# Optimization experiments

Hardware: AMD Instinct MI355X
Metric: run time of the kernel (lower is better)

Reference implementation:

```python
import jax, jax.numpy as jnp
import numpy as np

N_STOCKS = 5
SPD_DIM = N_STOCKS * (N_STOCKS + 1) // 2  # 15
STATE_DIM = N_STOCKS * N_STOCKS           # 25
CTX_DIM = 64
HIDDEN = 128
N_STEPS = 5
DT = 0.2
DIFFUSION_SCALE = 1.0
B = 4096
T = 32


def _spd_basis(n):
    bs = []
    for i in range(n):
        e = np.zeros((n, n), np.float32); e[i, i] = 1.0; bs.append(e)
    for i in range(n):
        for j in range(i + 1, n):
            e = np.zeros((n, n), np.float32)
            e[i, j] = e[j, i] = 1.0 / np.sqrt(2.0)
            bs.append(e)
    return jnp.asarray(np.stack(bs))  # (d, n, n) orthonormal symmetric basis

BASIS = _spd_basis(N_STOCKS)


def _sym(x):
    return 0.5 * (x + jnp.swapaxes(x, -1, -2))


def setup_inputs() -> dict:
    key = jax.random.key(0)
    ks = jax.random.split(key, 20)
    S, C, H, D = STATE_DIM, CTX_DIM, HIDDEN, SPD_DIM
    raw = jax.random.normal(ks[0], (B, T, N_STOCKS, N_STOCKS), jnp.float32)
    context_spd = raw @ jnp.swapaxes(raw, -1, -2) / N_STOCKS + jnp.eye(N_STOCKS, dtype=jnp.float32)
    dW = jax.random.normal(ks[1], (B, N_STEPS, D), jnp.float32) * jnp.sqrt(DT).astype(jnp.float32)

    def lin(k, out_d, in_d, scale=1.0):
        return jax.random.normal(k, (out_d, in_d), jnp.float32) * (scale / np.sqrt(in_d))

    inp_d = S + C  # 89
    return {
        "context_spd": context_spd,
        "dW": dW,
        "gru_wih": lin(ks[2], 3 * H, S),
        "gru_whh": lin(ks[3], 3 * H, H),
        "gru_bias": jnp.zeros((3 * H,), jnp.float32),
        "gru_bias_n": jnp.zeros((H,), jnp.float32),
        "proj_w": lin(ks[4], C, H),
        "proj_b": jnp.zeros((C,), jnp.float32),
        "drift_w0": lin(ks[5], H, inp_d), "drift_b0": jnp.zeros((H,), jnp.float32),
        "drift_w1": lin(ks[6], H, H),    "drift_b1": jnp.zeros((H,), jnp.float32),
        "drift_w2": lin(ks[7], H, H),    "drift_b2": jnp.zeros((H,), jnp.float32),
        "drift_w3": lin(ks[8], D, H) * 0.001, "drift_b3": jnp.zeros((D,), jnp.float32),
        "diff_w0": lin(ks[9], H, inp_d), "diff_b0": jnp.zeros((H,), jnp.float32),
        "diff_w1": lin(ks[10], H, H),   "diff_b1": jnp.zeros((H,), jnp.float32),
        "diff_w2": lin(ks[11], D, H) * 0.001, "diff_b2": jnp.full((D,), -3.0, jnp.float32),
    }


def reference(context_spd, dW, gru_wih, gru_whh, gru_bias, gru_bias_n, proj_w, proj_b,
              drift_w0, drift_b0, drift_w1, drift_b1, drift_w2, drift_b2, drift_w3, drift_b3,
              diff_w0, diff_b0, diff_w1, diff_b1, diff_w2, diff_b2):
    b = context_spd.shape[0]
    n = context_spd.shape[-1]

    # ---- GRU encoder over flattened symmetrized SPD matrices ----
    feats = _sym(context_spd).reshape(b, context_spd.shape[1], n * n)  # (B, T, S)

    def gru_step(h, x):  # x: (B, S), h: (B, H)
        gi = x @ gru_wih.T + gru_bias
        gh = h @ gru_whh.T
        ir, iz, ig = jnp.split(gi, 3, axis=-1)
        hr, hz, hg = jnp.split(gh, 3, axis=-1)
        r = jax.nn.sigmoid(ir + hr)
        z = jax.nn.sigmoid(iz + hz)
        g = jnp.tanh(ig + r * (hg + gru_bias_n))
        return (1.0 - z) * g + z * h, None

    h0 = jnp.zeros((b, gru_whh.shape[1]), feats.dtype)
    hT, _ = jax.lax.scan(gru_step, h0, jnp.swapaxes(feats, 0, 1))
    ctx = hT @ proj_w.T + proj_b  # (B, ctx_dim)

    # ---- SPD geometry helpers (affine-invariant frame) ----
    def sqrtm_sym(sig):
        w, v = jnp.linalg.eigh(sig)
        w = jnp.clip(w, 1e-8, None)
        return (v * jnp.sqrt(w)[..., None, :]) @ jnp.swapaxes(v, -1, -2)

    def expm_sym(a):
        w, v = jnp.linalg.eigh(a)
        return (v * jnp.exp(w)[..., None, :]) @ jnp.swapaxes(v, -1, -2)

    # ---- geometric Euler-Maruyama SDE step ----
    def sde_step(sigma, dw):  # sigma: (B,n,n), dw: (B,d)
        state = _sym(sigma).reshape(b, -1)
        inp = jnp.concatenate([state, ctx], axis=-1)  # (B, 89)
        # drift MLP (depth 3: 4 linears, silu)
        h = jax.nn.silu(inp @ drift_w0.T + drift_b0)
        h = jax.nn.silu(h @ drift_w1.T + drift_b1)
        h = jax.nn.silu(h @ drift_w2.T + drift_b2)
        drift_c = h @ drift_w3.T + drift_b3  # (B, d)
        # diffusion MLP (depth 2: 3 linears, silu), softplus-scaled
        g = jax.nn.silu(inp @ diff_w0.T + diff_b0)
        g = jax.nn.silu(g @ diff_w1.T + diff_b1)
        scales = jax.nn.softplus(g @ diff_w2.T + diff_b2) * DIFFUSION_SCALE  # (B, d)
        coeff = drift_c * DT + scales * dw  # tangent coordinates in orthonormal frame
        a = jnp.einsum('bk,kij->bij', coeff, BASIS)  # symmetric (B,n,n)
        L = sqrtm_sym(_sym(sigma))  # symmetric sqrt; frame E_k = L B_k L
        sigma_new = L @ expm_sym(a) @ L  # exp map: L expm(L^-1 V L^-1) L
        return _sym(sigma_new), None

    y0 = _sym(context_spd[:, -1])
    yT, _ = jax.lax.scan(sde_step, y0, jnp.swapaxes(dW, 0, 1))
    return _sym(yT)
```

## Files before the change

kernel.cpp:

```cpp
#include <hip/hip_runtime.h>
#include <hip/hip_bf16.h>

typedef unsigned int uint;

#define T_STEPS 32

#define OFF_WB    0
#define OFF_PJB   30720
#define OFF_D0B   34816
#define OFF_D1B   40960
#define OFF_D2B   49152
#define OFF_G0B   57344
#define OFF_G1B   63488
#define OFF_W3B   71680
#define OFF_G2B   72704

typedef _Float16 half8 __attribute__((ext_vector_type(8)));
typedef float    f32x4 __attribute__((ext_vector_type(4)));

union FB { uint4 u4; half8 h; };

__device__ inline uint pack2f(float a, float b) {
  _Float16 ha = (_Float16)a, hb = (_Float16)b;
  unsigned short ua, ub;
  __builtin_memcpy(&ua, &ha, 2);
  __builtin_memcpy(&ub, &hb, 2);
  return (uint)ua | ((uint)ub << 16);
}

__device__ inline float sigm(float x) { return 1.f / (1.f + __expf(-x)); }
__device__ inline float tanh_f(float x) {
  float ax = fabsf(x);
  float e = __expf(2.f * ax);
  float t = 1.f - 2.f / (e + 1.f);
  return copysignf(t, x);
}
__device__ inline float silu_f(float x) { return x / (1.f + __expf(-x)); }

__device__ inline float map89(const float* __restrict__ W, int u, int k) {
  if (k < 25) return W[u * 89 + k];
  if (k < 32) return 0.f;
  return W[u * 89 + k - 7];
}

__global__ __launch_bounds__(256) void prep_kernel(
    const float* __restrict__ wih, const float* __restrict__ whh,
    const float* __restrict__ pw,
    const float* __restrict__ dw0, const float* __restrict__ dw1,
    const float* __restrict__ dw2, const float* __restrict__ gw0,
    const float* __restrict__ gw1, const float* __restrict__ dw3,
    const float* __restrict__ gw2, uint* __restrict__ wsu) {
  int id = blockIdx.x * 256 + threadIdx.x;
  if (id < 30720) {
    int i = id & 3, l = (id >> 2) & 63, t3 = id >> 8;
    int kt = t3 % 5, wg = t3 / 5;
    int w = wg / 3, gi = wg % 3;
    int row = gi * 128 + w * 16 + (l & 15);
    int k = ((l >> 4) << 3) + i * 2;
    float a, b;
    if (kt == 0) {
      a = (k     < 25) ? wih[row * 25 + k]     : 0.f;
      b = (k + 1 < 25) ? wih[row * 25 + k + 1] : 0.f;
    } else {
      int kh = (kt - 1) * 32 + k;
      a = whh[row * 128 + kh];
      b = whh[row * 128 + kh + 1];
    }
    wsu[OFF_WB + id] = pack2f(a, b);
  } else if (id < 34816) {
    int t = id - 30720;
    int i = t & 3, l = (t >> 2) & 63, wkt = t >> 8;
    int kt = wkt & 3, w = wkt >> 2;
    int u = w * 16 + (l & 15);
    int k = kt * 32 + ((l >> 4) << 3) + i * 2;
    wsu[OFF_PJB + t] = pack2f(pw[u * 128 + k], pw[u * 128 + k + 1]);
  } else if (id < 40960) {
    int t = id - 34816;
    int i = t & 3, l = (t >> 2) & 63, wkt = t >> 8;
    int kt = wkt % 3, w = wkt / 3;
    int u = w * 16 + (l & 15);
    int k = kt * 32 + ((l >> 4) << 3) + i * 2;
    wsu[OFF_D0B + t] = pack2f(map89(dw0, u, k), map89(dw0, u, k + 1));
  } else if (id < 49152) {
    int t = id - 40960;
    int i = t & 3, l = (t >> 2) & 63, wkt = t >> 8;
    int kt = wkt & 3, w = wkt >> 2;
    int u = w * 16 + (l & 15);
    int k = kt * 32 + ((l >> 4) << 3) + i * 2;
    wsu[OFF_D1B + t] = pack2f(dw1[u * 128 + k], dw1[u * 128 + k + 1]);
  } else if (id < 57344) {
    int t = id - 49152;
    int i = t & 3, l = (t >> 2) & 63, wkt = t >> 8;
    int kt = wkt & 3, w = wkt >> 2;
    int u = w * 16 + (l & 15);
    int k = kt * 32 + ((l >> 4) << 3) + i * 2;
    wsu[OFF_D2B + t] = pack2f(dw2[u * 128 + k], dw2[u * 128 + k + 1]);
  } else if (id < 63488) {
    int t = id - 57344;
    int i = t & 3, l = (t >> 2) & 63, wkt = t >> 8;
    int kt = wkt % 3, w = wkt / 3;
    int u = w * 16 + (l & 15);
    int k = kt * 32 + ((l >> 4) << 3) + i * 2;
    wsu[OFF_G0B + t] = pack2f(map89(gw0, u, k), map89(gw0, u, k + 1));
  } else if (id < 71680) {
    int t = id - 63488;
    int i = t & 3, l = (t >> 2) & 63, wkt = t >> 8;
    int kt = wkt & 3, w = wkt >> 2;
    int u = w * 16 + (l & 15);
    int k = kt * 32 + ((l >> 4) << 3) + i * 2;
    wsu[OFF_G1B + t] = pack2f(gw1[u * 128 + k], gw1[u * 128 + k + 1]);
  } else if (id < 72704) {
    int t = id - 71680;
    int i = t & 3, l = (t >> 2) & 63, kt = t >> 8;
    int o = l & 15;
    int k = kt * 32 + ((l >> 4) << 3) + i * 2;
    float a = (o < 15) ? dw3[o * 128 + k]     : 0.f;
    float b = (o < 15) ? dw3[o * 128 + k + 1] : 0.f;
    wsu[OFF_W3B + t] = pack2f(a, b);
  } else if (id < 73728) {
    int t = id - 72704;
    int i = t & 3, l = (t >> 2) & 63, kt = t >> 8;
    int o = l & 15;
    int k = kt * 32 + ((l >> 4) << 3) + i * 2;
    float a = (o < 15) ? gw2[o * 128 + k]     : 0.f;
    float b = (o < 15) ? gw2[o * 128 + k + 1] : 0.f;
    wsu[OFF_G2B + t] = pack2f(a, b);
  }
}

template <int KT>
__device__ inline void mlp_pair(const _Float16* __restrict__ aA,
                                const FB* B0, const FB* B1,
                                float bias0, float bias1,
                                _Float16* __restrict__ outA,
                                int lm, int lq, int ubase) {
  f32x4 c0 = {0.f, 0.f, 0.f, 0.f}, c1 = {0.f, 0.f, 0.f, 0.f};
#pragma unroll
  for (int kt = 0; kt < KT; kt++) {
    half8 a = *(const half8*)(aA + ((kt * 4 + lq) * 16 + lm) * 8);
    c0 = __builtin_amdgcn_mfma_f32_16x16x32_f16(a, B0[kt].h, c0, 0, 0, 0);
    c1 = __builtin_amdgcn_mfma_f32_16x16x32_f16(a, B1[kt].h, c1, 0, 0, 0);
  }
  int u0 = ubase + lm, u1 = ubase + 16 + lm;
  int base0 = (u0 >> 3) * 128 + (u0 & 7);
  int base1 = (u1 >> 3) * 128 + (u1 & 7);
#pragma unroll
  for (int s = 0; s < 4; s++) {
    outA[base0 + (lq * 4 + s) * 8] = (_Float16)silu_f(c0[s] + bias0);
    outA[base1 + (lq * 4 + s) * 8] = (_Float16)silu_f(c1[s] + bias1);
  }
}

__device__ inline f32x4 head4(const _Float16* __restrict__ aA, const FB* H,
                              int lm, int lq) {
  f32x4 c = {0.f, 0.f, 0.f, 0.f};
#pragma unroll
  for (int kt = 0; kt < 4; kt++) {
    half8 a = *(const half8*)(aA + ((kt * 4 + lq) * 16 + lm) * 8);
    c = __builtin_amdgcn_mfma_f32_16x16x32_f16(a, H[kt].h, c, 0, 0, 0);
  }
  return c;
}

__device__ inline float bpf(int addr, float v) {
  return __int_as_float(__builtin_amdgcn_ds_bpermute(addr, __float_as_int(v)));
}
__device__ inline float mm5b(int iA, int iB, float A, float B) {
  float c = 0.f;
#pragma unroll
  for (int k = 0; k < 5; k++)
    c = fmaf(bpf(iA + 4 * k, A), bpf(iB + 20 * k, B), c);
  return c;
}

#define NS_ITER do { \
  float P_  = mm5b(iA0, iB0, Zv, Yv); \
  float Tm_ = 1.5f * gdel - 0.5f * P_; \
  float Yn_ = mm5b(iA0, iB0, Yv, Tm_); \
  float Zn_ = mm5b(iA0, iB0, Tm_, Zv); \
  Yv = Yn_; Zv = Zn_; } while (0)

__global__ __launch_bounds__(512) void fused_kernel(
    const float* __restrict__ ctp, const float* __restrict__ dWp,
    const uint* __restrict__ wsu,
    const float* __restrict__ gbias, const float* __restrict__ gbn,
    const float* __restrict__ projb,
    const float* __restrict__ db0, const float* __restrict__ db1,
    const float* __restrict__ db2, const float* __restrict__ b3,
    const float* __restrict__ gb0, const float* __restrict__ gb1,
    const float* __restrict__ gb2, float* __restrict__ outp) {
  __shared__ __align__(16) _Float16 bigbuf[16384];
  __shared__ __align__(16) _Float16 hf[2][4][4][16][8];
  __shared__ float sig_s[16 * 28];
  __shared__ float coeff_s[256];
  __shared__ float coeff2_s[256];
  const int tid = threadIdx.x;
  const int rb = blockIdx.x * 16;
  uint* bigu = (uint*)bigbuf;

  for (int idx = tid; idx < T_STEPS * 16 * 16; idx += 512) {
    int k2 = idx & 15, r = (idx >> 4) & 15, t = idx >> 8;
    const float* base = ctp + ((rb + r) * T_STEPS + t) * 25;
    int k0 = 2 * k2;
    float v0 = 0.f, v1 = 0.f;
    if (k0 < 25)     { int i5 = k0 / 5,     j5 = k0 % 5;     v0 = 0.5f * (base[i5*5+j5] + base[j5*5+i5]); }
    if (k0 + 1 < 25) { int i5 = (k0+1) / 5, j5 = (k0+1) % 5; v1 = 0.5f * (base[i5*5+j5] + base[j5*5+i5]); }
    int q = k2 >> 2, jh = k2 & 3;
    bigu[((t * 4 + q) * 16 + r) * 4 + jh] = pack2f(v0, v1);
  }

  const int w = tid >> 6, l = tid & 63;
  const int lm = l & 15, lq = l >> 4;
  const int u = w * 16 + lm;
  const int ku = u >> 5, qu = (u >> 3) & 3, ju = u & 7;
  FB Bf[3][5];
  const uint4* wb4p = (const uint4*)(wsu + OFF_WB);
#pragma unroll
  for (int gi = 0; gi < 3; gi++)
#pragma unroll
    for (int kt = 0; kt < 5; kt++)
      Bf[gi][kt].u4 = wb4p[((w * 3 + gi) * 5 + kt) * 64 + l];
  const float br = gbias[u], bz = gbias[128 + u], bg = gbias[256 + u], bn = gbn[u];
  float hprev[4] = {0.f, 0.f, 0.f, 0.f};
  __syncthreads();

  f32x4 z4 = {0.f, 0.f, 0.f, 0.f};
  half8 axn = *(const half8*)(bigbuf + ((0 * 4 + lq) * 16 + lm) * 8);
  f32x4 pxr = __builtin_amdgcn_mfma_f32_16x16x32_f16(axn, Bf[0][0].h, z4, 0, 0, 0);
  f32x4 pxz = __builtin_amdgcn_mfma_f32_16x16x32_f16(axn, Bf[1][0].h, z4, 0, 0, 0);
  f32x4 pxg = __builtin_amdgcn_mfma_f32_16x16x32_f16(axn, Bf[2][0].h, z4, 0, 0, 0);
  for (int t = 0; t < T_STEPS; t++) {
    f32x4 cr = pxr, cz = pxz, cgv = pxg;
    f32x4 ch = {0.f, 0.f, 0.f, 0.f};
    if (t > 0) {
      const int p = t & 1;
#pragma unroll
      for (int kk = 0; kk < 4; kk++) {
        half8 ah = *(const half8*)(&hf[p][kk][lq][lm][0]);
        cr = __builtin_amdgcn_mfma_f32_16x16x32_f16(ah, Bf[0][1 + kk].h, cr, 0, 0, 0);
        cz = __builtin_amdgcn_mfma_f32_16x16x32_f16(ah, Bf[1][1 + kk].h, cz, 0, 0, 0);
        ch = __builtin_amdgcn_mfma_f32_16x16x32_f16(ah, Bf[2][1 + kk].h, ch, 0, 0, 0);
      }
    }
    if (t < T_STEPS - 1) {
      axn = *(const half8*)(bigbuf + (((t + 1) * 4 + lq) * 16 + lm) * 8);
      pxr = __builtin_amdgcn_mfma_f32_16x16x32_f16(axn, Bf[0][0].h, z4, 0, 0, 0);
      pxz = __builtin_amdgcn_mfma_f32_16x16x32_f16(axn, Bf[1][0].h, z4, 0, 0, 0);
      pxg = __builtin_amdgcn_mfma_f32_16x16x32_f16(axn, Bf[2][0].h, z4, 0, 0, 0);
    }
    const int wp = (t + 1) & 1;
#pragma unroll
    for (int s = 0; s < 4; s++) {
      float r = sigm(cr[s] + br);
      float z = sigm(cz[s] + bz);
      float g = tanh_f(cgv[s] + bg + r * (ch[s] + bn));
      float hn = (1.f - z) * g + z * hprev[s];
      hprev[s] = hn;
      hf[wp][ku][qu][lq * 4 + s][ju] = (_Float16)hn;
    }
    __syncthreads();
  }

  const int role = w >> 2;
  const int wbq = w & 3;
  FB F0[2][3], F1[2][4], F2[2][4], Pf[4], Hf[4];
  {
    const uint4* p0 = (const uint4*)(wsu + (role ? OFF_G0B : OFF_D0B));
    const uint4* p1 = (const uint4*)(wsu + (role ? OFF_G1B : OFF_D1B));
    const uint4* p2 = (const uint4*)(wsu + (role ? OFF_G1B : OFF_D2B));
#pragma unroll
    for (int s = 0; s < 2; s++) {
      int slot = wbq * 2 + s;
#pragma unroll
      for (int kt = 0; kt < 3; kt++) F0[s][kt].u4 = p0[(slot * 3 + kt) * 64 + l];
#pragma unroll
      for (int kt = 0; kt < 4; kt++) {
        F1[s][kt].u4 = p1[(slot * 4 + kt) * 64 + l];
        F2[s][kt].u4 = p2[(slot * 4 + kt) * 64 + l];
      }
    }
  }
  if (w < 4) {
#pragma unroll
    for (int kt = 0; kt < 4; kt++)
      Pf[kt].u4 = ((const uint4*)(wsu + OFF_PJB))[(w * 4 + kt) * 64 + l];
  }
  if (w == 0) {
#pragma unroll
    for (int kt = 0; kt < 4; kt++)
      Hf[kt].u4 = ((const uint4*)(wsu + OFF_W3B))[kt * 64 + l];
  } else if (w == 4) {
#pragma unroll
    for (int kt = 0; kt < 4; kt++)
      Hf[kt].u4 = ((const uint4*)(wsu + OFF_G2B))[kt * 64 + l];
  }
  float b0s[2], b1s[2], b2s[2];
#pragma unroll
  for (int s = 0; s < 2; s++) {
    int us = wbq * 32 + s * 16 + lm;
    b0s[s] = role ? gb0[us] : db0[us];
    b1s[s] = role ? gb1[us] : db1[us];
    b2s[s] = role ? 0.f : db2[us];
  }
  const int oc = (lm < 15) ? lm : 0;
  const float hb = (w == 0) ? b3[oc] : ((w == 4) ? gb2[oc] : 0.f);

  _Float16* inpA = bigbuf;
  _Float16* bufA = bigbuf + 1536;
  _Float16* bufB = bigbuf + 3584;
  _Float16* bufC = bigbuf + 5632;
  _Float16* bufD = bigbuf + 7680;

  if (w < 4) {
    f32x4 c = {0.f, 0.f, 0.f, 0.f};
#pragma unroll
    for (int kt = 0; kt < 4; kt++) {
      half8 a = *(const half8*)(&hf[0][kt][lq][lm][0]);
      c = __builtin_amdgcn_mfma_f32_16x16x32_f16(a, Pf[kt].h, c, 0, 0, 0);
    }
    const float pbv = projb[u];
    int kk = 32 + u, base = (kk >> 3) * 128 + (kk & 7);
#pragma unroll
    for (int s = 0; s < 4; s++)
      inpA[base + (lq * 4 + s) * 8] = (_Float16)(c[s] + pbv);
  }
  for (int idx = tid; idx < 400; idx += 512) {
    int e = idx / 25, k = idx % 25;
    int i5 = k / 5, j5 = k % 5;
    const float* base = ctp + ((rb + e) * T_STEPS + 31) * 25;
    float v = 0.5f * (base[i5 * 5 + j5] + base[j5 * 5 + i5]);
    sig_s[e * 28 + k] = v;
    inpA[(k >> 3) * 128 + e * 8 + (k & 7)] = (_Float16)v;
  }
  if (tid < 112) {
    int e = tid / 7, p = 25 + tid % 7;
    inpA[(p >> 3) * 128 + e * 8 + (p & 7)] = (_Float16)0.f;
  }
  const int ge = tid >> 5, glane = tid & 31;
  const int gli = (glane < 25) ? glane : 0;
  const int gii = gli / 5, gjj = gli % 5;
  const float gdel = (gii == gjj) ? 1.f : 0.f;
  const int gbase = (l & 32) << 2;
  const int iA0 = gbase + gii * 20;
  const int iB0 = gbase + gjj * 4;
  const int iT0 = gbase + (gjj * 5 + gii) * 4;
  __syncthreads();

  for (int st = 0; st < 5; st++) {
    float S = sig_s[ge * 28 + gli];
    float tr = 0.f;
#pragma unroll
    for (int d = 0; d < 5; d++) tr += bpf(gbase + 24 * d, S);
    const float That = S * (2.298851f / tr) - 1.068966f * gdel;
    float dwv[4] = {0.f, 0.f, 0.f, 0.f};
    if (w == 4) {
#pragma unroll
      for (int s = 0; s < 4; s++)
        dwv[s] = dWp[((rb + lq * 4 + s) * 5 + st) * 15 + oc];
    }
    float Yv, Zv;
    mlp_pair<3>(inpA, F0[0], F0[1], b0s[0], b0s[1], role ? bufB : bufA, lm, lq, wbq * 32);
    {
      float T2 = mm5b(iA0, iB0, That, That);
      float X  = -1.13859f * That + 0.9901f * T2;
      float Zp = mm5b(iA0, iB0, T2, X)
               + 1.03702f * gdel - 0.21179f * That + 0.09756f * T2;
      Zv = Zp;
      float TZ = mm5b(iA0, iB0, That, Zp);
      Yv = 0.87f * TZ + 0.93f * Zp;
    }
    __syncthreads();
    mlp_pair<4>(role ? bufB : bufA, F1[0], F1[1], b1s[0], b1s[1],
                role ? bufD : bufC, lm, lq, wbq * 32);
    NS_ITER;
    __syncthreads();
    if (!role) {
      mlp_pair<4>(bufC, F2[0], F2[1], b2s[0], b2s[1], bufA, lm, lq, wbq * 32);
    } else if (w == 4) {
      f32x4 c = head4(bufD, Hf, lm, lq);
      if (lm < 15) {
#pragma unroll
        for (int s = 0; s < 4; s++) {
          float acc = c[s] + hb;
          float sp = (acc > 20.f) ? acc : __logf(1.f + __expf(acc));
          coeff2_s[(lq * 4 + s) * 16 + lm] = sp * dwv[s];
        }
      }
    }
    NS_ITER;
    __syncthreads();
    if (w == 0) {
      f32x4 c = head4(bufA, Hf, lm, lq);
      if (lm < 15) {
#pragma unroll
        for (int s = 0; s < 4; s++)
          coeff_s[(lq * 4 + s) * 16 + lm] = 0.2f * (c[s] + hb);
      }
    }
    NS_ITER;
    float L = Yv * sqrtf(0.5f * tr);
    __syncthreads();
    {
      float av;
      if (gii == gjj) av = coeff_s[ge * 16 + gii] + coeff2_s[ge * 16 + gii];
      else {
        int p = gii < gjj ? gii : gjj, qq = gii < gjj ? gjj : gii;
        int i5 = 5 + (p * (9 - p)) / 2 + (qq - p - 1);
        av = (coeff_s[ge * 16 + i5] + coeff2_s[ge * 16 + i5]) * 0.70710678f;
      }
      float a2 = mm5b(iA0, iB0, av, av);
      float a3 = mm5b(iA0, iB0, a2, av);
      float q1 = gdel * 0.16666667f + av * 0.04166667f
               + a2 * 0.00833333f + a3 * 0.00138889f;
      float M = gdel + av + 0.5f * a2 + mm5b(iA0, iB0, a3, q1);
      float P2 = mm5b(iA0, iB0, L, M);
      float S2 = mm5b(iA0, iB0, P2, L);
      S2 = 0.5f * (S2 + bpf(iT0, S2));
      if (glane < 25) {
        sig_s[ge * 28 + gli] = S2;
        inpA[(gli >> 3) * 128 + ge * 8 + (gli & 7)] = (_Float16)S2;
      }
    }
    __syncthreads();
  }

  for (int idx = tid; idx < 400; idx += 512) {
    int e = idx / 25, k = idx % 25;
    outp[(rb + e) * 25 + k] = sig_s[e * 28 + k];
  }
}

extern "C" void kernel_launch(void* const* d_in, const int* in_sizes, int n_in,
                              void* d_out, int out_size, void* d_ws, size_t ws_size,
                              hipStream_t stream) {
  const float* ctp = (const float*)d_in[0];
  const float* dWp = (const float*)d_in[1];
  const float* wih = (const float*)d_in[2];
  const float* whh = (const float*)d_in[3];
  const float* gb  = (const float*)d_in[4];
  const float* gbn = (const float*)d_in[5];
  const float* pw  = (const float*)d_in[6];
  const float* pb  = (const float*)d_in[7];
  const float* dw0 = (const float*)d_in[8];
  const float* db0 = (const float*)d_in[9];
  const float* dw1 = (const float*)d_in[10];
  const float* db1 = (const float*)d_in[11];
  const float* dw2 = (const float*)d_in[12];
  const float* db2 = (const float*)d_in[13];
  const float* dw3 = (const float*)d_in[14];
  const float* db3 = (const float*)d_in[15];
  const float* gw0 = (const float*)d_in[16];
  const float* gb0 = (const float*)d_in[17];
  const float* gw1 = (const float*)d_in[18];
  const float* gb1 = (const float*)d_in[19];
  const float* gw2 = (const float*)d_in[20];
  const float* gb2 = (const float*)d_in[21];
  uint* wsu = (uint*)d_ws;

  hipLaunchKernelGGL(prep_kernel, dim3(288), dim3(256), 0, stream,
                     wih, whh, pw, dw0, dw1, dw2, gw0, gw1, dw3, gw2, wsu);
  hipLaunchKernelGGL(fused_kernel, dim3(256), dim3(512), 0, stream,
                     ctp, dWp, wsu, gb, gbn, pb,
                     db0, db1, db2, db3, gb0, gb1, gb2, (float*)d_out);
}
```

Baseline: 174.8 us.

## Split fused kernel into GRU and SDE kernels, halve SDE tile, use dot2 heads

The single fused kernel is split in two. A GRU kernel keeps 16 rows per 512-thread block and writes the fp16 context projection to workspace. A new SDE kernel runs 8 rows per 256-thread block over twice as many blocks, with each wave computing four output slices instead of two. The small drift and diffusion output heads now use packed fp16 dot2 instructions from weights held in LDS, replacing the single-wave MFMA heads, and one barrier is removed. The aim is better CU occupancy and less serial head work in the SDE phase, at the cost of an extra launch, a global round trip for the context, and more registers per wave.

```diff
diff --git a/kernel.cpp b/kernel.cpp
--- a/kernel.cpp
+++ b/kernel.cpp
@@ -12,9 +12,11 @@
 #define OFF_D2B   49152
 #define OFF_G0B   57344
 #define OFF_G1B   63488
-#define OFF_W3B   71680
-#define OFF_G2B   72704
-
+#define OFF_W3P   71680
+#define OFF_G2P   72640
+#define OFF_CTXG  73600
+
+typedef _Float16 h2v  __attribute__((ext_vector_type(2)));
 typedef _Float16 half8 __attribute__((ext_vector_type(8)));
 typedef float    f32x4 __attribute__((ext_vector_type(4)));
 
@@ -27,6 +29,22 @@
   __builtin_memcpy(&ub, &hb, 2);
   return (uint)ua | ((uint)ub << 16);
 }
+
+__device__ inline float dot2(uint w, uint a, float acc) {
+#if __has_builtin(__builtin_amdgcn_fdot2)
+  union U { uint u; h2v h; };
+  U uw, ua; uw.u = w; ua.u = a;
+  return __builtin_amdgcn_fdot2(uw.h, ua.h, acc, false);
+#else
+  union U { uint u; _Float16 h[2]; };
+  U uw, ua; uw.u = w; ua.u = a;
+  return acc + (float)uw.h[0] * (float)ua.h[0] + (float)uw.h[1] * (float)ua.h[1];
+#endif
+}
+
+#define DOT4(accv, wv, xv)                                             \
+  accv = dot2((wv).x, (xv).x, accv); accv = dot2((wv).y, (xv).y, accv);\
+  accv = dot2((wv).z, (xv).z, accv); accv = dot2((wv).w, (xv).w, accv);
 
 __device__ inline float sigm(float x) { return 1.f / (1.f + __expf(-x)); }
 __device__ inline float tanh_f(float x) {
@@ -109,94 +127,26 @@
     int u = w * 16 + (l & 15);
     int k = kt * 32 + ((l >> 4) << 3) + i * 2;
     wsu[OFF_G1B + t] = pack2f(gw1[u * 128 + k], gw1[u * 128 + k + 1]);
-  } else if (id < 72704) {
+  } else if (id < 72640) {
     int t = id - 71680;
-    int i = t & 3, l = (t >> 2) & 63, kt = t >> 8;
-    int o = l & 15;
-    int k = kt * 32 + ((l >> 4) << 3) + i * 2;
-    float a = (o < 15) ? dw3[o * 128 + k]     : 0.f;
-    float b = (o < 15) ? dw3[o * 128 + k + 1] : 0.f;
-    wsu[OFF_W3B + t] = pack2f(a, b);
-  } else if (id < 73728) {
-    int t = id - 72704;
-    int i = t & 3, l = (t >> 2) & 63, kt = t >> 8;
-    int o = l & 15;
-    int k = kt * 32 + ((l >> 4) << 3) + i * 2;
-    float a = (o < 15) ? gw2[o * 128 + k]     : 0.f;
-    float b = (o < 15) ? gw2[o * 128 + k + 1] : 0.f;
-    wsu[OFF_G2B + t] = pack2f(a, b);
-  }
-}
-
-template <int KT>
-__device__ inline void mlp_pair(const _Float16* __restrict__ aA,
-                                const FB* B0, const FB* B1,
-                                float bias0, float bias1,
-                                _Float16* __restrict__ outA,
-                                int lm, int lq, int ubase) {
-  f32x4 c0 = {0.f, 0.f, 0.f, 0.f}, c1 = {0.f, 0.f, 0.f, 0.f};
-#pragma unroll
-  for (int kt = 0; kt < KT; kt++) {
-    half8 a = *(const half8*)(aA + ((kt * 4 + lq) * 16 + lm) * 8);
-    c0 = __builtin_amdgcn_mfma_f32_16x16x32_f16(a, B0[kt].h, c0, 0, 0, 0);
-    c1 = __builtin_amdgcn_mfma_f32_16x16x32_f16(a, B1[kt].h, c1, 0, 0, 0);
-  }
-  int u0 = ubase + lm, u1 = ubase + 16 + lm;
-  int base0 = (u0 >> 3) * 128 + (u0 & 7);
-  int base1 = (u1 >> 3) * 128 + (u1 & 7);
-#pragma unroll
-  for (int s = 0; s < 4; s++) {
-    outA[base0 + (lq * 4 + s) * 8] = (_Float16)silu_f(c0[s] + bias0);
-    outA[base1 + (lq * 4 + s) * 8] = (_Float16)silu_f(c1[s] + bias1);
-  }
-}
-
-__device__ inline f32x4 head4(const _Float16* __restrict__ aA, const FB* H,
-                              int lm, int lq) {
-  f32x4 c = {0.f, 0.f, 0.f, 0.f};
-#pragma unroll
-  for (int kt = 0; kt < 4; kt++) {
-    half8 a = *(const half8*)(aA + ((kt * 4 + lq) * 16 + lm) * 8);
-    c = __builtin_amdgcn_mfma_f32_16x16x32_f16(a, H[kt].h, c, 0, 0, 0);
-  }
-  return c;
-}
-
-__device__ inline float bpf(int addr, float v) {
-  return __int_as_float(__builtin_amdgcn_ds_bpermute(addr, __float_as_int(v)));
-}
-__device__ inline float mm5b(int iA, int iB, float A, float B) {
-  float c = 0.f;
-#pragma unroll
-  for (int k = 0; k < 5; k++)
-    c = fmaf(bpf(iA + 4 * k, A), bpf(iB + 20 * k, B), c);
-  return c;
-}
-
-#define NS_ITER do { \
-  float P_  = mm5b(iA0, iB0, Zv, Yv); \
-  float Tm_ = 1.5f * gdel - 0.5f * P_; \
-  float Yn_ = mm5b(iA0, iB0, Yv, Tm_); \
-  float Zn_ = mm5b(iA0, iB0, Tm_, Zv); \
-  Yv = Yn_; Zv = Zn_; } while (0)
-
-__global__ __launch_bounds__(512) void fused_kernel(
-    const float* __restrict__ ctp, const float* __restrict__ dWp,
-    const uint* __restrict__ wsu,
+    int o = t >> 6, k2 = t & 63;
+    wsu[OFF_W3P + t] = pack2f(dw3[o * 128 + 2 * k2], dw3[o * 128 + 2 * k2 + 1]);
+  } else if (id < 73600) {
+    int t = id - 72640;
+    int o = t >> 6, k2 = t & 63;
+    wsu[OFF_G2P + t] = pack2f(gw2[o * 128 + 2 * k2], gw2[o * 128 + 2 * k2 + 1]);
+  }
+}
+
+__global__ __launch_bounds__(512) void gru_kernel(
+    const float* __restrict__ ctp, const uint* __restrict__ wsu,
     const float* __restrict__ gbias, const float* __restrict__ gbn,
-    const float* __restrict__ projb,
-    const float* __restrict__ db0, const float* __restrict__ db1,
-    const float* __restrict__ db2, const float* __restrict__ b3,
-    const float* __restrict__ gb0, const float* __restrict__ gb1,
-    const float* __restrict__ gb2, float* __restrict__ outp) {
-  __shared__ __align__(16) _Float16 bigbuf[16384];
+    const float* __restrict__ projb, _Float16* __restrict__ ctxg) {
+  __shared__ __align__(16) _Float16 x2[T_STEPS][4][16][8];
   __shared__ __align__(16) _Float16 hf[2][4][4][16][8];
-  __shared__ float sig_s[16 * 28];
-  __shared__ float coeff_s[256];
-  __shared__ float coeff2_s[256];
   const int tid = threadIdx.x;
   const int rb = blockIdx.x * 16;
-  uint* bigu = (uint*)bigbuf;
+  uint* x2u = (uint*)x2;
 
   for (int idx = tid; idx < T_STEPS * 16 * 16; idx += 512) {
     int k2 = idx & 15, r = (idx >> 4) & 15, t = idx >> 8;
@@ -206,7 +156,7 @@
     if (k0 < 25)     { int i5 = k0 / 5,     j5 = k0 % 5;     v0 = 0.5f * (base[i5*5+j5] + base[j5*5+i5]); }
     if (k0 + 1 < 25) { int i5 = (k0+1) / 5, j5 = (k0+1) % 5; v1 = 0.5f * (base[i5*5+j5] + base[j5*5+i5]); }
     int q = k2 >> 2, jh = k2 & 3;
-    bigu[((t * 4 + q) * 16 + r) * 4 + jh] = pack2f(v0, v1);
+    x2u[((t * 4 + q) * 16 + r) * 4 + jh] = pack2f(v0, v1);
   }
 
   const int w = tid >> 6, l = tid & 63;
@@ -225,7 +175,7 @@
   __syncthreads();
 
   f32x4 z4 = {0.f, 0.f, 0.f, 0.f};
-  half8 axn = *(const half8*)(bigbuf + ((0 * 4 + lq) * 16 + lm) * 8);
+  half8 axn = *(const half8*)(&x2[0][lq][lm][0]);
   f32x4 pxr = __builtin_amdgcn_mfma_f32_16x16x32_f16(axn, Bf[0][0].h, z4, 0, 0, 0);
   f32x4 pxz = __builtin_amdgcn_mfma_f32_16x16x32_f16(axn, Bf[1][0].h, z4, 0, 0, 0);
   f32x4 pxg = __builtin_amdgcn_mfma_f32_16x16x32_f16(axn, Bf[2][0].h, z4, 0, 0, 0);
@@ -243,7 +193,7 @@
       }
     }
     if (t < T_STEPS - 1) {
-      axn = *(const half8*)(bigbuf + (((t + 1) * 4 + lq) * 16 + lm) * 8);
+      axn = *(const half8*)(&x2[t + 1][lq][lm][0]);
       pxr = __builtin_amdgcn_mfma_f32_16x16x32_f16(axn, Bf[0][0].h, z4, 0, 0, 0);
       pxz = __builtin_amdgcn_mfma_f32_16x16x32_f16(axn, Bf[1][0].h, z4, 0, 0, 0);
       pxg = __builtin_amdgcn_mfma_f32_16x16x32_f16(axn, Bf[2][0].h, z4, 0, 0, 0);
@@ -261,16 +211,124 @@
     __syncthreads();
   }
 
-  const int role = w >> 2;
-  const int wbq = w & 3;
-  FB F0[2][3], F1[2][4], F2[2][4], Pf[4], Hf[4];
+  if (w < 4) {
+    FB Pf[4];
+#pragma unroll
+    for (int kt = 0; kt < 4; kt++)
+      Pf[kt].u4 = ((const uint4*)(wsu + OFF_PJB))[(w * 4 + kt) * 64 + l];
+    f32x4 c = {0.f, 0.f, 0.f, 0.f};
+#pragma unroll
+    for (int kt = 0; kt < 4; kt++) {
+      half8 a = *(const half8*)(&hf[0][kt][lq][lm][0]);
+      c = __builtin_amdgcn_mfma_f32_16x16x32_f16(a, Pf[kt].h, c, 0, 0, 0);
+    }
+    const float pbv = projb[u];
+#pragma unroll
+    for (int s = 0; s < 4; s++)
+      ctxg[(rb + lq * 4 + s) * 64 + u] = (_Float16)(c[s] + pbv);
+  }
+}
+
+template <int KT>
+__device__ inline void mlp_pair(const _Float16* __restrict__ aA,
+                                const FB* B0, const FB* B1,
+                                float bias0, float bias1,
+                                _Float16* __restrict__ outA,
+                                int lm, int lq, int ubase) {
+  f32x4 c0 = {0.f, 0.f, 0.f, 0.f}, c1 = {0.f, 0.f, 0.f, 0.f};
+#pragma unroll
+  for (int kt = 0; kt < KT; kt++) {
+    half8 a = *(const half8*)(aA + ((kt * 4 + lq) * 16 + lm) * 8);
+    c0 = __builtin_amdgcn_mfma_f32_16x16x32_f16(a, B0[kt].h, c0, 0, 0, 0);
+    c1 = __builtin_amdgcn_mfma_f32_16x16x32_f16(a, B1[kt].h, c1, 0, 0, 0);
+  }
+  int u0 = ubase + lm, u1 = ubase + 16 + lm;
+  int base0 = (u0 >> 3) * 128 + (u0 & 7);
+  int base1 = (u1 >> 3) * 128 + (u1 & 7);
+#pragma unroll
+  for (int s = 0; s < 4; s++) {
+    outA[base0 + (lq * 4 + s) * 8] = (_Float16)silu_f(c0[s] + bias0);
+    outA[base1 + (lq * 4 + s) * 8] = (_Float16)silu_f(c1[s] + bias1);
+  }
+}
+
+__device__ inline float bpf(int addr, float v) {
+  return __int_as_float(__builtin_amdgcn_ds_bpermute(addr, __float_as_int(v)));
+}
+__device__ inline float mm5b(int iA, int iB, float A, float B) {
+  float c = 0.f;
+#pragma unroll
+  for (int k = 0; k < 5; k++)
+    c = fmaf(bpf(iA + 4 * k, A), bpf(iB + 20 * k, B), c);
+  return c;
+}
+
+#define NS_ITER do { \
+  float P_  = mm5b(iA0, iB0, Zv, Yv); \
+  float Tm_ = 1.5f * gdel - 0.5f * P_; \
+  float Yn_ = mm5b(iA0, iB0, Yv, Tm_); \
+  float Zn_ = mm5b(iA0, iB0, Tm_, Zv); \
+  Yv = Yn_; Zv = Zn_; } while (0)
+
+__global__ __launch_bounds__(256, 2) void sde_kernel(
+    const float* __restrict__ ctp, const float* __restrict__ dWp,
+    const uint* __restrict__ wsu,
+    const float* __restrict__ db0, const float* __restrict__ db1,
+    const float* __restrict__ db2, const float* __restrict__ b3,
+    const float* __restrict__ gb0, const float* __restrict__ gb1,
+    const float* __restrict__ gb2, float* __restrict__ outp) {
+  __shared__ __align__(16) _Float16 abuf[1536 + 4 * 2048];
+  __shared__ __align__(16) uint w3s[15 * 68 + 4];
+  __shared__ __align__(16) uint gw2s[15 * 68 + 4];
+  __shared__ float sig_s[8 * 28];
+  __shared__ float coeff_s[128];
+  __shared__ float coeff2_s[128];
+  const int tid = threadIdx.x;
+  const int eb = blockIdx.x * 8;
+  _Float16* inpA = abuf;
+  _Float16* bufA = abuf + 1536;
+  _Float16* bufB = abuf + 3584;
+  _Float16* bufC = abuf + 5632;
+  _Float16* bufD = abuf + 7680;
+  const int w = tid >> 6, l = tid & 63;
+  const int lm = l & 15, lq = l >> 4;
+  const int role = w >> 1, wq = w & 1;
+
+  for (int i = tid; i < 960; i += 256) {
+    int o = i >> 6, k2 = i & 63;
+    w3s[o * 68 + k2]  = wsu[OFF_W3P + i];
+    gw2s[o * 68 + k2] = wsu[OFF_G2P + i];
+  }
+  const _Float16* ctxh = (const _Float16*)(wsu + OFF_CTXG);
+  for (int idx = tid; idx < 512; idx += 256) {
+    int e = idx >> 6, c = idx & 63, k = 32 + c;
+    inpA[(k >> 3) * 128 + e * 8 + (k & 7)] = ctxh[(eb + e) * 64 + c];
+  }
+  for (int idx = tid; idx < 768; idx += 256) {
+    int c16 = idx >> 6, rem = idx & 63;
+    inpA[c16 * 128 + (8 + (rem >> 3)) * 8 + (rem & 7)] = (_Float16)0.f;
+  }
+  for (int idx = tid; idx < 200; idx += 256) {
+    int e = idx / 25, k = idx % 25;
+    int i5 = k / 5, j5 = k % 5;
+    const float* base = ctp + ((eb + e) * T_STEPS + 31) * 25;
+    float v = 0.5f * (base[i5 * 5 + j5] + base[j5 * 5 + i5]);
+    sig_s[e * 28 + k] = v;
+    inpA[(k >> 3) * 128 + e * 8 + (k & 7)] = (_Float16)v;
+  }
+  if (tid < 56) {
+    int e = tid / 7, p = 25 + tid % 7;
+    inpA[(p >> 3) * 128 + e * 8 + (p & 7)] = (_Float16)0.f;
+  }
+
+  FB F0[4][3], F1[4][4], F2[4][4];
   {
     const uint4* p0 = (const uint4*)(wsu + (role ? OFF_G0B : OFF_D0B));
     const uint4* p1 = (const uint4*)(wsu + (role ? OFF_G1B : OFF_D1B));
     const uint4* p2 = (const uint4*)(wsu + (role ? OFF_G1B : OFF_D2B));
 #pragma unroll
-    for (int s = 0; s < 2; s++) {
-      int slot = wbq * 2 + s;
+    for (int s = 0; s < 4; s++) {
+      int slot = wq * 4 + s;
 #pragma unroll
       for (int kt = 0; kt < 3; kt++) F0[s][kt].u4 = p0[(slot * 3 + kt) * 64 + l];
 #pragma unroll
@@ -280,62 +338,15 @@
       }
     }
   }
-  if (w < 4) {
-#pragma unroll
-    for (int kt = 0; kt < 4; kt++)
-      Pf[kt].u4 = ((const uint4*)(wsu + OFF_PJB))[(w * 4 + kt) * 64 + l];
-  }
-  if (w == 0) {
-#pragma unroll
-    for (int kt = 0; kt < 4; kt++)
-      Hf[kt].u4 = ((const uint4*)(wsu + OFF_W3B))[kt * 64 + l];
-  } else if (w == 4) {
-#pragma unroll
-    for (int kt = 0; kt < 4; kt++)
-      Hf[kt].u4 = ((const uint4*)(wsu + OFF_G2B))[kt * 64 + l];
-  }
-  float b0s[2], b1s[2], b2s[2];
-#pragma unroll
-  for (int s = 0; s < 2; s++) {
-    int us = wbq * 32 + s * 16 + lm;
+  float b0s[4], b1s[4], b2s[4];
+#pragma unroll
+  for (int s = 0; s < 4; s++) {
+    int us = wq * 64 + s * 16 + lm;
     b0s[s] = role ? gb0[us] : db0[us];
     b1s[s] = role ? gb1[us] : db1[us];
     b2s[s] = role ? 0.f : db2[us];
   }
-  const int oc = (lm < 15) ? lm : 0;
-  const float hb = (w == 0) ? b3[oc] : ((w == 4) ? gb2[oc] : 0.f);
-
-  _Float16* inpA = bigbuf;
-  _Float16* bufA = bigbuf + 1536;
-  _Float16* bufB = bigbuf + 3584;
-  _Float16* bufC = bigbuf + 5632;
-  _Float16* bufD = bigbuf + 7680;
-
-  if (w < 4) {
-    f32x4 c = {0.f, 0.f, 0.f, 0.f};
-#pragma unroll
-    for (int kt = 0; kt < 4; kt++) {
-      half8 a = *(const half8*)(&hf[0][kt][lq][lm][0]);
-      c = __builtin_amdgcn_mfma_f32_16x16x32_f16(a, Pf[kt].h, c, 0, 0, 0);
-    }
-    const float pbv = projb[u];
-    int kk = 32 + u, base = (kk >> 3) * 128 + (kk & 7);
-#pragma unroll
-    for (int s = 0; s < 4; s++)
-      inpA[base + (lq * 4 + s) * 8] = (_Float16)(c[s] + pbv);
-  }
-  for (int idx = tid; idx < 400; idx += 512) {
-    int e = idx / 25, k = idx % 25;
-    int i5 = k / 5, j5 = k % 5;
-    const float* base = ctp + ((rb + e) * T_STEPS + 31) * 25;
-    float v = 0.5f * (base[i5 * 5 + j5] + base[j5 * 5 + i5]);
-    sig_s[e * 28 + k] = v;
-    inpA[(k >> 3) * 128 + e * 8 + (k & 7)] = (_Float16)v;
-  }
-  if (tid < 112) {
-    int e = tid / 7, p = 25 + tid % 7;
-    inpA[(p >> 3) * 128 + e * 8 + (p & 7)] = (_Float16)0.f;
-  }
+
   const int ge = tid >> 5, glane = tid & 31;
   const int gli = (glane < 25) ? glane : 0;
   const int gii = gli / 5, gjj = gli % 5;
@@ -344,6 +355,8 @@
   const int iA0 = gbase + gii * 20;
   const int iB0 = gbase + gjj * 4;
   const int iT0 = gbase + (gjj * 5 + gii) * 4;
+  const float b3r = (glane < 15) ? b3[glane] : 0.f;
+  const float g2r = (glane < 15) ? gb2[glane] : 0.f;
   __syncthreads();
 
   for (int st = 0; st < 5; st++) {
@@ -352,14 +365,10 @@
 #pragma unroll
     for (int d = 0; d < 5; d++) tr += bpf(gbase + 24 * d, S);
     const float That = S * (2.298851f / tr) - 1.068966f * gdel;
-    float dwv[4] = {0.f, 0.f, 0.f, 0.f};
-    if (w == 4) {
-#pragma unroll
-      for (int s = 0; s < 4; s++)
-        dwv[s] = dWp[((rb + lq * 4 + s) * 5 + st) * 15 + oc];
-    }
+    float dwv = (glane < 15) ? dWp[((eb + ge) * 5 + st) * 15 + glane] : 0.f;
     float Yv, Zv;
-    mlp_pair<3>(inpA, F0[0], F0[1], b0s[0], b0s[1], role ? bufB : bufA, lm, lq, wbq * 32);
+    mlp_pair<3>(inpA, F0[0], F0[1], b0s[0], b0s[1], role ? bufB : bufA, lm, lq, wq * 64);
+    mlp_pair<3>(inpA, F0[2], F0[3], b0s[2], b0s[3], role ? bufB : bufA, lm, lq, wq * 64 + 32);
     {
       float T2 = mm5b(iA0, iB0, That, That);
       float X  = -1.13859f * That + 0.9901f * T2;
@@ -371,35 +380,34 @@
     }
     __syncthreads();
     mlp_pair<4>(role ? bufB : bufA, F1[0], F1[1], b1s[0], b1s[1],
-                role ? bufD : bufC, lm, lq, wbq * 32);
+                role ? bufD : bufC, lm, lq, wq * 64);
+    mlp_pair<4>(role ? bufB : bufA, F1[2], F1[3], b1s[2], b1s[3],
+                role ? bufD : bufC, lm, lq, wq * 64 + 32);
     NS_ITER;
     __syncthreads();
     if (!role) {
-      mlp_pair<4>(bufC, F2[0], F2[1], b2s[0], b2s[1], bufA, lm, lq, wbq * 32);
-    } else if (w == 4) {
-      f32x4 c = head4(bufD, Hf, lm, lq);
-      if (lm < 15) {
-#pragma unroll
-        for (int s = 0; s < 4; s++) {
-          float acc = c[s] + hb;
-          float sp = (acc > 20.f) ? acc : __logf(1.f + __expf(acc));
-          coeff2_s[(lq * 4 + s) * 16 + lm] = sp * dwv[s];
-        }
-      }
+      mlp_pair<4>(bufC, F2[0], F2[1], b2s[0], b2s[1], bufA, lm, lq, wq * 64);
+      mlp_pair<4>(bufC, F2[2], F2[3], b2s[2], b2s[3], bufA, lm, lq, wq * 64 + 32);
     }
     NS_ITER;
     __syncthreads();
-    if (w == 0) {
-      f32x4 c = head4(bufA, Hf, lm, lq);
-      if (lm < 15) {
-#pragma unroll
-        for (int s = 0; s < 4; s++)
-          coeff_s[(lq * 4 + s) * 16 + lm] = 0.2f * (c[s] + hb);
+    if (glane < 15) {
+      float accD = b3r, accG = g2r;
+      const uint4* w3r = (const uint4*)(w3s + glane * 68);
+      const uint4* g2rr = (const uint4*)(gw2s + glane * 68);
+#pragma unroll
+      for (int c = 0; c < 16; c++) {
+        uint4 avD = *(const uint4*)((const uint*)(bufA + c * 128 + ge * 8));
+        uint4 avG = *(const uint4*)((const uint*)(bufD + c * 128 + ge * 8));
+        DOT4(accD, w3r[c], avD);
+        DOT4(accG, g2rr[c], avG);
       }
+      coeff_s[ge * 16 + glane] = 0.2f * accD;
+      float sp = (accG > 20.f) ? accG : __logf(1.f + __expf(accG));
+      coeff2_s[ge * 16 + glane] = sp * dwv;
     }
     NS_ITER;
     float L = Yv * sqrtf(0.5f * tr);
-    __syncthreads();
     {
       float av;
       if (gii == gjj) av = coeff_s[ge * 16 + gii] + coeff2_s[ge * 16 + gii];
@@ -424,9 +432,9 @@
     __syncthreads();
   }
 
-  for (int idx = tid; idx < 400; idx += 512) {
+  for (int idx = tid; idx < 200; idx += 256) {
     int e = idx / 25, k = idx % 25;
-    outp[(rb + e) * 25 + k] = sig_s[e * 28 + k];
+    outp[(eb + e) * 25 + k] = sig_s[e * 28 + k];
   }
 }
 
@@ -456,10 +464,13 @@
   const float* gw2 = (const float*)d_in[20];
   const float* gb2 = (const float*)d_in[21];
   uint* wsu = (uint*)d_ws;
+  _Float16* ctxg = (_Float16*)(wsu + OFF_CTXG);
 
   hipLaunchKernelGGL(prep_kernel, dim3(288), dim3(256), 0, stream,
                      wih, whh, pw, dw0, dw1, dw2, gw0, gw1, dw3, gw2, wsu);
-  hipLaunchKernelGGL(fused_kernel, dim3(256), dim3(512), 0, stream,
-                     ctp, dWp, wsu, gb, gbn, pb,
-                     db0, db1, db2, db3, gb0, gb1, gb2, (float*)d_out);
-}
+  hipLaunchKernelGGL(gru_kernel, dim3(256), dim3(512), 0, stream,
+                     ctp, wsu, gb, gbn, pb, ctxg);
+  hipLaunchKernelGGL(sde_kernel, dim3(512), dim3(256), 0, stream,
+                     ctp, dWp, wsu, db0, db1, db2, db3,
+                     gb0, gb1, gb2, (float*)d_out);
+}
```

Result: slower. 200.0 us (+14.4%).
